# Kernel optimization log

Measured on AMD Instinct MI355X. Metric: run time of the kernel, lower is better.

Reference implementation:

```python
import jax, jax.numpy as jnp
import numpy as np

N_HEAD, D_MODEL, DQ, DK, DV = 16, 1024, 64, 64, 64
B, LQ, LK = 2, 2048, 2048
EPS = 1e-3


def setup_inputs() -> dict:
    key = jax.random.key(0)
    ks = jax.random.split(key, 8)
    v = jax.random.normal(ks[0], (B, LK, D_MODEL), jnp.float32)
    k = jax.random.normal(ks[1], (B, LK, D_MODEL), jnp.float32)
    q = jax.random.normal(ks[2], (B, LQ, D_MODEL), jnp.float32)
    mask = jax.random.randint(ks[3], (B, LQ, LK), 0, 2).astype(bool)
    # xavier_normal for [n_head, d_model, d*]: fan_in=d_model, fan_out=d* (per torch, last two dims)
    def xav(kk, shape):
        std = np.sqrt(2.0 / (shape[-2] + shape[-1]))
        return jax.random.normal(kk, shape, jnp.float32) * std
    w_q = xav(ks[4], (N_HEAD, D_MODEL, DQ))
    w_k = xav(ks[5], (N_HEAD, D_MODEL, DK))
    w_v = xav(ks[6], (N_HEAD, D_MODEL, DV))
    # output linear: torch default init; use uniform(-1/sqrt(fan_in), ..)
    fan_in = N_HEAD * DV
    bound = 1.0 / np.sqrt(fan_in)
    kw, kb = jax.random.split(ks[7])
    w_o = jax.random.uniform(kw, (fan_in, D_MODEL), jnp.float32, -bound, bound)
    b_o = jax.random.uniform(kb, (D_MODEL,), jnp.float32, -bound, bound)
    gamma = jnp.ones((D_MODEL,), jnp.float32)
    beta = jnp.zeros((D_MODEL,), jnp.float32)
    return {"v": v, "k": k, "q": q, "mask": mask, "w_q": w_q, "w_k": w_k,
            "w_v": w_v, "w_o": w_o, "b_o": b_o, "gamma": gamma, "beta": beta}


def _layer_norm(x, gamma, beta):
    mean = jnp.mean(x, axis=-1, keepdims=True)
    # torch.std default is unbiased (ddof=1); eps added to std (not var)
    std = jnp.std(x, axis=-1, keepdims=True, ddof=1)
    return (x - mean) / (std + EPS) * gamma + beta


def reference(v, k, q, mask, w_q, w_k, w_v, w_o, b_o, gamma, beta):
    residual = k  # source uses k as residual
    # per-head projections: [h, b, l, d*]
    qh = jnp.einsum('bld,hde->hble', q, w_q)
    kh = jnp.einsum('bld,hde->hble', k, w_k)
    vh = jnp.einsum('bld,hde->hble', v, w_v)
    scale = 1.0 / np.sqrt(DK)
    scores = jnp.einsum('hbqe,hbke->hbqk', qh, kh) * scale  # [h,b,Lq,Lk]
    scores = jnp.where(mask[None], -jnp.inf, scores)
    attn = jax.nn.softmax(scores, axis=-1)
    out = jnp.einsum('hbqk,hbke->hbqe', attn, vh)  # [h,b,Lq,dv]
    # cat(split(out, batch, dim=0), dim=-1): heads concatenated on last dim
    out = out.transpose(1, 2, 0, 3).reshape(out.shape[1], out.shape[2], -1)
    out = out @ w_o + b_o
    x = out + residual  # dropout is identity in eval
    return _layer_norm(x, gamma, beta)
```

## Files before the change

### kernel.cpp

```cpp
#include <hip/hip_runtime.h>
#include <math.h>

typedef __bf16 bf16_t;
typedef bf16_t bf16x8 __attribute__((ext_vector_type(8)));
typedef float  f32x4  __attribute__((ext_vector_type(4)));
typedef unsigned short u16;
typedef u16 ushortx4 __attribute__((ext_vector_type(4)));
typedef unsigned long long u64;

#define MFMA16(a, b, c) __builtin_amdgcn_mfma_f32_16x16x32_bf16((a), (b), (c), 0, 0, 0)

__device__ __forceinline__ u16 f2bf(float f) {
    unsigned int u = __float_as_uint(f);
    u = (u + 0x7fffu + ((u >> 16) & 1u)) >> 16;
    return (u16)u;
}

__device__ __forceinline__ float bf2f(unsigned int u) {
    return __uint_as_float(u << 16);
}

__device__ __forceinline__ void gld16(const u16* g, u16* l) {
    __builtin_amdgcn_global_load_lds(
        (const __attribute__((address_space(1))) void*)g,
        (__attribute__((address_space(3))) void*)l, 16, 0, 0);
}


__global__ __launch_bounds__(256) void k_prep(const float* __restrict__ q,
                                              const float* __restrict__ k,
                                              const float* __restrict__ v,
                                              const int* __restrict__ mask,
                                              const float* __restrict__ w_q,
                                              const float* __restrict__ w_k,
                                              const float* __restrict__ w_v,
                                              const float* __restrict__ w_o,
                                              u16* __restrict__ qb,
                                              u16* __restrict__ kb,
                                              u16* __restrict__ vb,
                                              u64* __restrict__ mask64,
                                              u16* __restrict__ wqt,
                                              u16* __restrict__ wkt,
                                              u16* __restrict__ wvt,
                                              u16* __restrict__ wot) {
    __shared__ float tile[32][33];
    int bid = blockIdx.x;
    if (bid < 12288) {
        int sel = bid >> 12;
        int i = (bid & 4095) * 256 + threadIdx.x;
        const float* src = sel == 0 ? q : (sel == 1 ? k : v);
        u16* dst = sel == 0 ? qb : (sel == 1 ? kb : vb);
        float4 val = ((const float4*)src)[i];
        ushortx4 r;
        r[0] = f2bf(val.x); r[1] = f2bf(val.y); r[2] = f2bf(val.z); r[3] = f2bf(val.w);
        ((ushortx4*)dst)[i] = r;
    } else if (bid < 20480) {
        int b2 = bid - 12288;
        int ktg = b2 & 7, q4 = (b2 >> 3) & 511, b = b2 >> 12;
        int wave = threadIdx.x >> 6, lane = threadIdx.x & 63;
        int qq = q4 * 4 + wave;
        const int* mp = mask + ((size_t)(b * 2048 + qq)) * 2048 + ktg * 256 + lane;
#pragma unroll
        for (int i = 0; i < 4; ++i) {
            int m = mp[i * 64];
            u64 bal = __ballot(m != 0);
            if (lane == 0) mask64[((size_t)(b * 32 + ktg * 4 + i)) * 2048 + qq] = bal;
        }
    } else {
        int b3 = bid - 20480;
        const float* src;
        u16* dst;
        int r0, c0, C;
        if (b3 < 3072) {
            int x = b3 & 31, y = (b3 >> 5) & 1, z = b3 >> 6;
            int h = z & 15, sel = z >> 4;
            src = (sel == 0 ? w_q : (sel == 1 ? w_k : w_v)) + (size_t)h * 65536;
            dst = (sel == 0 ? wqt : (sel == 1 ? wkt : wvt)) + (size_t)h * 65536;
            r0 = x * 32; c0 = y * 32; C = 64;
        } else {
            int t = b3 - 3072;
            r0 = (t & 31) * 32; c0 = (t >> 5) * 32; C = 1024;
            src = w_o; dst = wot;
        }
        int tx = threadIdx.x & 31, ty = threadIdx.x >> 5;
        const float* s = src + ((size_t)r0) * C + c0;
#pragma unroll
        for (int i = 0; i < 4; ++i) tile[ty + i * 8][tx] = s[(ty + i * 8) * (size_t)C + tx];
        __syncthreads();
        u16* d = dst + ((size_t)c0) * 1024 + r0;
#pragma unroll
        for (int i = 0; i < 4; ++i) d[(ty + i * 8) * 1024 + tx] = f2bf(tile[tx][ty + i * 8]);
    }
}

#define GEMM_CORE(Ablk, Bblk, ACC)                                                    \
    int c0 = wave * 2;                                                                \
    const u16* Ag0 = Ablk + (size_t)(c0 * 16 + l15) * 1024 + quad * 8;                \
    const u16* Ag1 = Ablk + (size_t)((c0 + 1) * 16 + l15) * 1024 + quad * 8;          \
    const u16* Bg0 = Bblk + (size_t)(c0 * 16 + l15) * 1024 + quad * 8;                \
    const u16* Bg1 = Bblk + (size_t)((c0 + 1) * 16 + l15) * 1024 + quad * 8;          \
    gld16(Ag0, As + c0 * 512); gld16(Ag1, As + (c0 + 1) * 512);                       \
    gld16(Bg0, Bs + c0 * 512); gld16(Bg1, Bs + (c0 + 1) * 512);                       \
    __syncthreads();                                                                  \
    int buf = 0;                                                                      \
    for (int ks = 0; ks < 32; ++ks) {                                                 \
        if (ks < 31) {                                                                \
            int k0 = (ks + 1) * 32;                                                   \
            gld16(Ag0 + k0, As + (buf ^ 1) * 4096 + c0 * 512);                        \
            gld16(Ag1 + k0, As + (buf ^ 1) * 4096 + (c0 + 1) * 512);                  \
            gld16(Bg0 + k0, Bs + (buf ^ 1) * 4096 + c0 * 512);                        \
            gld16(Bg1 + k0, Bs + (buf ^ 1) * 4096 + (c0 + 1) * 512);                  \
        }                                                                             \
        bf16x8 af[4], bfr[4];                                                         \
        _Pragma("unroll")                                                             \
        for (int i = 0; i < 4; ++i)                                                   \
            af[i] = *(const bf16x8*)(As + buf * 4096 + (wy * 4 + i) * 512 + lane * 8);\
        _Pragma("unroll")                                                             \
        for (int j = 0; j < 4; ++j)                                                   \
            bfr[j] = *(const bf16x8*)(Bs + buf * 4096 + (wx * 4 + j) * 512 + lane * 8);\
        _Pragma("unroll")                                                             \
        for (int i = 0; i < 4; ++i)                                                   \
            _Pragma("unroll")                                                         \
            for (int j = 0; j < 4; ++j) ACC[i][j] = MFMA16(af[i], bfr[j], ACC[i][j]); \
        __syncthreads();                                                              \
        buf ^= 1;                                                                     \
    }

__global__ __launch_bounds__(256) void k_proj(
    const u16* __restrict__ qb, const u16* __restrict__ kb, const u16* __restrict__ vb,
    const u16* __restrict__ wqt, const u16* __restrict__ wkt, const u16* __restrict__ wvt,
    u16* __restrict__ oq, u16* __restrict__ okh, u16* __restrict__ ovt) {
    __shared__ __align__(16) u16 smem[18432];
    u16* As = smem;
    u16* Bs = smem + 8192;
    int z = blockIdx.y, gx = blockIdx.x;
    int bm, bn;
    const u16 *A, *B;
    if (z == 0)      { bm = gx & 31; bn = gx >> 5; A = qb; B = wqt; }
    else if (z == 1) { bm = gx & 31; bn = gx >> 5; A = kb; B = wkt; }
    else             { bn = gx & 31; bm = gx >> 5; A = wvt; B = vb; }
    A += (size_t)bm * 128 * 1024;
    B += (size_t)bn * 128 * 1024;
    int tid = threadIdx.x, wave = tid >> 6, lane = tid & 63;
    int wy = wave >> 1, wx = wave & 1, l15 = lane & 15, quad = lane >> 4;
    f32x4 acc[4][4] = {};
    GEMM_CORE(A, B, acc)
    u16* ep = smem + wave * 4608;
    float mulf = (z == 0) ? 0.18033688011112042f : 1.0f;
#pragma unroll
    for (int i = 0; i < 4; ++i)
#pragma unroll
        for (int j = 0; j < 4; ++j)
#pragma unroll
            for (int r = 0; r < 4; ++r)
                ep[(i * 16 + quad * 4 + r) * 72 + j * 16 + l15] = f2bf(acc[i][j][r] * mulf);
    int rl = lane >> 3, cg = lane & 7;
    if (z < 2) {
        int hh = bn * 2 + wx;
        int m0 = bm * 128 + wy * 64;
        int bb = m0 >> 11, l0 = m0 & 2047;
        u16* O = (z ? okh : oq) + ((size_t)((hh * 2 + bb) * 2048 + l0)) * 64;
#pragma unroll
        for (int s = 0; s < 8; ++s) {
            int row = s * 8 + rl;
            uint4 v = *(const uint4*)(ep + row * 72 + cg * 8);
            *(uint4*)(O + (size_t)row * 64 + cg * 8) = v;
        }
    } else {
        int m0 = bm * 128 + wy * 64;
        int hh = m0 >> 6;
        int n0 = bn * 128 + wx * 64;
        int bb = n0 >> 11, l0 = n0 & 2047;
        u16* O = ovt + (size_t)(hh * 2 + bb) * 131072 + (size_t)(m0 & 63) * 2048 + l0;
#pragma unroll
        for (int s = 0; s < 8; ++s) {
            int row = s * 8 + rl;
            uint4 v = *(const uint4*)(ep + row * 72 + cg * 8);
            *(uint4*)(O + (size_t)row * 2048 + cg * 8) = v;
        }
    }
}

__global__ __launch_bounds__(256) void k_attn(
    const u16* __restrict__ qh, const u16* __restrict__ kh,
    const u16* __restrict__ vt, const u64* __restrict__ mask64,
    u16* __restrict__ po, float* __restrict__ pl) {
    int hb = blockIdx.x, qt = blockIdx.y, ksp = blockIdx.z;
    int b = hb & 1;
    int tid = threadIdx.x, wave = tid >> 6, lane = tid & 63;
    int l15 = lane & 15, quad = lane >> 4;

    __shared__ __align__(16) u16 Ks[2][4096], Vs[2][4096];
    __shared__ __align__(16) u16 Eb[4][1024];

    int qrow0 = qt * 128 + wave * 32;
    const u16* Qp = qh + ((size_t)(hb * 2048) + qrow0 + l15) * 64 + quad * 8;
    bf16x8 qf[2][2];
    qf[0][0] = *(const bf16x8*)Qp;
    qf[0][1] = *(const bf16x8*)(Qp + 32);
    qf[1][0] = *(const bf16x8*)(Qp + 1024);
    qf[1][1] = *(const bf16x8*)(Qp + 1024 + 32);

    int c0 = wave * 2;
    int rowp = (wave >> 1) * 32 + (l15 >> 2) * 8 + (wave & 1) * 4 + (l15 & 3);
    const u16* Kg0 = kh + (size_t)hb * 131072 + (size_t)ksp * 65536 +
                     (size_t)rowp * 64 + quad * 8;
    const u16* Kg1 = Kg0 + 32;
    const u16* Vg0 = vt + (size_t)hb * 131072 + (size_t)(wave * 16 + l15) * 2048 +
                     ksp * 1024 + quad * 8;
    const u16* Vg1 = Vg0 + 32;
    const u64* Mp = mask64 + (size_t)b * 65536 + (size_t)ksp * 32768 + qrow0 + l15;

    float l_lane[2] = {0.f, 0.f};
    f32x4 o[2][4] = {};

    gld16(Kg0, &Ks[0][c0 * 512]);
    gld16(Kg1, &Ks[0][(c0 + 1) * 512]);
    gld16(Vg0, &Vs[0][c0 * 512]);
    gld16(Vg1, &Vs[0][(c0 + 1) * 512]);
    u64 mw0 = Mp[0], mw1 = Mp[16];
    __syncthreads();
    int buf = 0;
    for (int kt = 0; kt < 16; ++kt) {
        u64 mwn0 = 0, mwn1 = 0;
        if (kt < 15) {
            gld16(Kg0 + (size_t)(kt + 1) * 4096, &Ks[buf ^ 1][c0 * 512]);
            gld16(Kg1 + (size_t)(kt + 1) * 4096, &Ks[buf ^ 1][(c0 + 1) * 512]);
            gld16(Vg0 + (size_t)(kt + 1) * 64, &Vs[buf ^ 1][c0 * 512]);
            gld16(Vg1 + (size_t)(kt + 1) * 64, &Vs[buf ^ 1][(c0 + 1) * 512]);
            mwn0 = Mp[(size_t)(kt + 1) * 2048];
            mwn1 = Mp[(size_t)(kt + 1) * 2048 + 16];
        }
        bf16x8 kf[8], vf[8];
#pragma unroll
        for (int c = 0; c < 8; ++c) kf[c] = *(const bf16x8*)&Ks[buf][c * 512 + lane * 8];
#pragma unroll
        for (int c = 0; c < 8; ++c) vf[c] = *(const bf16x8*)&Vs[buf][c * 512 + lane * 8];
#pragma unroll
        for (int hf = 0; hf < 2; ++hf) {
            u64 mw = hf ? mw1 : mw0;
            f32x4 st[4] = {};
#pragma unroll
            for (int t = 0; t < 4; ++t) {
                st[t] = MFMA16(kf[t * 2], qf[hf][0], st[t]);
                st[t] = MFMA16(kf[t * 2 + 1], qf[hf][1], st[t]);
            }
            unsigned int w0 = (unsigned int)(mw >> (quad * 8));
            unsigned int w1 = (unsigned int)(mw >> (32 + quad * 8));
#pragma unroll
            for (int r = 0; r < 4; ++r) {
                st[0][r] = ((w0 >> r) & 1u) ? -3e30f : st[0][r];
                st[1][r] = ((w0 >> (4 + r)) & 1u) ? -3e30f : st[1][r];
                st[2][r] = ((w1 >> r) & 1u) ? -3e30f : st[2][r];
                st[3][r] = ((w1 >> (4 + r)) & 1u) ? -3e30f : st[3][r];
            }
            float ll = 0.f;
            unsigned int pw[8];
#pragma unroll
            for (int t = 0; t < 4; ++t) {
                float p0 = __builtin_amdgcn_exp2f(st[t][0]);
                float p1 = __builtin_amdgcn_exp2f(st[t][1]);
                float p2 = __builtin_amdgcn_exp2f(st[t][2]);
                float p3 = __builtin_amdgcn_exp2f(st[t][3]);
                ll += (p0 + p1) + (p2 + p3);
                pw[t * 2]     = (__float_as_uint(p1) & 0xffff0000u) | (__float_as_uint(p0) >> 16);
                pw[t * 2 + 1] = (__float_as_uint(p3) & 0xffff0000u) | (__float_as_uint(p2) >> 16);
            }
            l_lane[hf] += ll;
            union { unsigned int w[4]; bf16x8 v; } p0u, p1u;
            p0u.w[0] = pw[0]; p0u.w[1] = pw[1]; p0u.w[2] = pw[2]; p0u.w[3] = pw[3];
            p1u.w[0] = pw[4]; p1u.w[1] = pw[5]; p1u.w[2] = pw[6]; p1u.w[3] = pw[7];
#pragma unroll
            for (int t = 0; t < 4; ++t) {
                o[hf][t] = MFMA16(p0u.v, vf[t * 2], o[hf][t]);
                o[hf][t] = MFMA16(p1u.v, vf[t * 2 + 1], o[hf][t]);
            }
        }
        mw0 = mwn0; mw1 = mwn1;
        __syncthreads();
        buf ^= 1;
    }
    size_t rowbase = ((size_t)ksp * 32 + hb) * 2048 + qrow0;
    int rl = lane >> 3, cg = lane & 7;
#pragma unroll
    for (int hf = 0; hf < 2; ++hf) {
        float ls = l_lane[hf];
        ls += __shfl_xor(ls, 16, 64);
        ls += __shfl_xor(ls, 32, 64);
        if (quad == 0) pl[rowbase + hf * 16 + l15] = ls;
#pragma unroll
        for (int t = 0; t < 4; ++t)
#pragma unroll
            for (int r = 0; r < 4; ++r) {
                int row = quad * 4 + r, col = t * 16 + l15;
                int g = col >> 3;
                Eb[wave][row * 64 + ((g ^ (row & 7)) << 3) + (col & 7)] =
                    f2bf(o[hf][t][r]);
            }
#pragma unroll
        for (int s = 0; s < 2; ++s) {
            int row = s * 8 + rl;
            uint4 v = *(const uint4*)&Eb[wave][row * 64 + ((cg ^ (row & 7)) << 3)];
            *(uint4*)(po + (rowbase + hf * 16 + row) * 64 + cg * 8) = v;
        }
    }
}

__global__ __launch_bounds__(256) void k_amerge(const u16* __restrict__ po,
                                                const float* __restrict__ pl,
                                                u16* __restrict__ ao) {
    int bid = blockIdx.x;
    int hb = bid >> 6, rc = bid & 63;
    int h = hb >> 1, b = hb & 1;
    int tid = threadIdx.x;
    int r = tid >> 3, c = tid & 7;
    int row = rc * 32 + r;
    size_t i0 = ((size_t)hb * 2048 + row) * 64 + c * 8;
    uint4 a0 = *(const uint4*)(po + i0);
    uint4 a1 = *(const uint4*)(po + i0 + 4194304);
    float l0 = pl[(size_t)hb * 2048 + row];
    float l1 = pl[65536 + (size_t)hb * 2048 + row];
    float inv = 1.0f / (l0 + l1);
    unsigned int* pa0 = (unsigned int*)&a0;
    unsigned int* pa1 = (unsigned int*)&a1;
    uint4 out;
    unsigned int* po_ = (unsigned int*)&out;
#pragma unroll
    for (int i = 0; i < 4; ++i) {
        float lo = (bf2f(pa0[i] & 0xffffu) + bf2f(pa1[i] & 0xffffu)) * inv;
        float hi = (bf2f(pa0[i] >> 16) + bf2f(pa1[i] >> 16)) * inv;
        po_[i] = (unsigned int)f2bf(lo) | ((unsigned int)f2bf(hi) << 16);
    }
    *(uint4*)(ao + ((size_t)(b * 2048 + row)) * 1024 + h * 64 + c * 8) = out;
}

__global__ __launch_bounds__(512) void k_out(
    const u16* __restrict__ ao, const u16* __restrict__ wot,
    float* __restrict__ xp0, float* __restrict__ xp1) {
    __shared__ __align__(16) u16 smem[18432];
    u16* As = smem;
    u16* Bs = smem + 8192;
    int gx = blockIdx.x, bm = gx & 31, bn = gx >> 5;
    int ksp = blockIdx.y;
    const u16* A = ao + (size_t)bm * 128 * 1024 + ksp * 512;
    const u16* B = wot + (size_t)bn * 128 * 1024 + ksp * 512;
    float* xp = ksp ? xp1 : xp0;
    int tid = threadIdx.x, wave = tid >> 6, lane = tid & 63;
    int wy = wave >> 2, wx = wave & 3, l15 = lane & 15, quad = lane >> 4;
    const u16* Ag = A + (size_t)(wave * 16 + l15) * 1024 + quad * 8;
    const u16* Bg = B + (size_t)(wave * 16 + l15) * 1024 + quad * 8;
    f32x4 acc[4][2] = {};
    gld16(Ag, As + wave * 512);
    gld16(Bg, Bs + wave * 512);
    __syncthreads();
    int buf = 0;
    for (int ks = 0; ks < 16; ++ks) {
        if (ks < 15) {
            int k0 = (ks + 1) * 32;
            gld16(Ag + k0, As + (buf ^ 1) * 4096 + wave * 512);
            gld16(Bg + k0, Bs + (buf ^ 1) * 4096 + wave * 512);
        }
        bf16x8 af[4], bfr[2];
#pragma unroll
        for (int i = 0; i < 4; ++i)
            af[i] = *(const bf16x8*)(As + buf * 4096 + (wy * 4 + i) * 512 + lane * 8);
#pragma unroll
        for (int j = 0; j < 2; ++j)
            bfr[j] = *(const bf16x8*)(Bs + buf * 4096 + (wx * 2 + j) * 512 + lane * 8);
#pragma unroll
        for (int i = 0; i < 4; ++i)
#pragma unroll
            for (int j = 0; j < 2; ++j) acc[i][j] = MFMA16(af[i], bfr[j], acc[i][j]);
        __syncthreads();
        buf ^= 1;
    }
    float* epf = (float*)smem + wave * 1152;
    int rl = lane >> 3, cg = lane & 7;
    int mbase = bm * 128 + wy * 64, nbase = bn * 128 + wx * 32;
#pragma unroll
    for (int cc = 0; cc < 2; ++cc) {
#pragma unroll
        for (int i2 = 0; i2 < 2; ++i2)
#pragma unroll
            for (int j = 0; j < 2; ++j)
#pragma unroll
                for (int r = 0; r < 4; ++r)
                    epf[(i2 * 16 + quad * 4 + r) * 36 + j * 16 + l15] =
                        acc[cc * 2 + i2][j][r];
#pragma unroll
        for (int s = 0; s < 4; ++s) {
            int row = s * 8 + rl;
            f32x4 v = *(const f32x4*)(epf + row * 36 + cg * 4);
            int m = mbase + cc * 32 + row, n = nbase + cg * 4;
            *(f32x4*)(xp + (size_t)m * 1024 + n) = v;
        }
    }
}

__global__ __launch_bounds__(256) void k_ln(const float* __restrict__ xp0,
                                            const float* __restrict__ xp1,
                                            const float* __restrict__ resid,
                                            const float* __restrict__ bo,
                                            const float* __restrict__ gamma,
                                            const float* __restrict__ beta,
                                            float* __restrict__ out) {
    int row = blockIdx.x;
    size_t base = (size_t)row * 256;
    float4 a0 = ((const float4*)xp0)[base + threadIdx.x];
    float4 a1 = ((const float4*)xp1)[base + threadIdx.x];
    float4 rs = ((const float4*)resid)[base + threadIdx.x];
    float4 b4 = ((const float4*)bo)[threadIdx.x];
    float4 v;
    v.x = a0.x + a1.x + rs.x + b4.x;
    v.y = a0.y + a1.y + rs.y + b4.y;
    v.z = a0.z + a1.z + rs.z + b4.z;
    v.w = a0.w + a1.w + rs.w + b4.w;
    float s = v.x + v.y + v.z + v.w;
    float ss = v.x * v.x + v.y * v.y + v.z * v.z + v.w * v.w;
#pragma unroll
    for (int off = 32; off; off >>= 1) {
        s += __shfl_down(s, off, 64);
        ss += __shfl_down(ss, off, 64);
    }
    __shared__ float sb[8];
    int wave = threadIdx.x >> 6, lane = threadIdx.x & 63;
    if (lane == 0) { sb[wave] = s; sb[4 + wave] = ss; }
    __syncthreads();
    s = sb[0] + sb[1] + sb[2] + sb[3];
    ss = sb[4] + sb[5] + sb[6] + sb[7];
    float mean = s * (1.0f / 1024.0f);
    float var = fmaxf((ss - 1024.0f * mean * mean) * (1.0f / 1023.0f), 0.f);
    float inv = 1.0f / (sqrtf(var) + 1e-3f);
    float4 g = ((const float4*)gamma)[threadIdx.x];
    float4 bt = ((const float4*)beta)[threadIdx.x];
    float4 o;
    o.x = (v.x - mean) * inv * g.x + bt.x;
    o.y = (v.y - mean) * inv * g.y + bt.y;
    o.z = (v.z - mean) * inv * g.z + bt.z;
    o.w = (v.w - mean) * inv * g.w + bt.w;
    ((float4*)(out))[base + threadIdx.x] = o;
}

extern "C" void kernel_launch(void* const* d_in, const int* in_sizes, int n_in,
                              void* d_out, int out_size, void* d_ws, size_t ws_size,
                              hipStream_t stream) {
    const float* v_in  = (const float*)d_in[0];
    const float* k_in  = (const float*)d_in[1];
    const float* q_in  = (const float*)d_in[2];
    const int*   mask  = (const int*)d_in[3];
    const float* w_q   = (const float*)d_in[4];
    const float* w_k   = (const float*)d_in[5];
    const float* w_v   = (const float*)d_in[6];
    const float* w_o   = (const float*)d_in[7];
    const float* b_o   = (const float*)d_in[8];
    const float* gamma = (const float*)d_in[9];
    const float* beta  = (const float*)d_in[10];
    float* out = (float*)d_out;

    char* ws = (char*)d_ws;
    const size_t MB = 1ull << 20;
    u16* qb  = (u16*)(ws + 0 * MB);
    u16* kb  = (u16*)(ws + 8 * MB);
    u16* vb  = (u16*)(ws + 16 * MB);
    u16* wqt = (u16*)(ws + 24 * MB);
    u16* wkt = (u16*)(ws + 26 * MB);
    u16* wvt = (u16*)(ws + 28 * MB);
    u16* wot = (u16*)(ws + 30 * MB);
    u16* qh  = (u16*)(ws + 32 * MB);
    u16* kh  = (u16*)(ws + 40 * MB);
    u16* vt  = (u16*)(ws + 48 * MB);
    u16* ao  = (u16*)(ws + 56 * MB);
    u64* mask64 = (u64*)(ws + 64 * MB);
    u16*   po = (u16*)(ws + 0 * MB);
    float* pl = (float*)(ws + 16 * MB);
    float* xp0 = (float*)(ws + 32 * MB);
    float* xp1 = (float*)(ws + 64 * MB);

    k_prep<<<dim3(24576), dim3(256), 0, stream>>>(q_in, k_in, v_in, mask,
                                                  w_q, w_k, w_v, w_o,
                                                  qb, kb, vb, mask64,
                                                  wqt, wkt, wvt, wot);
    k_proj<<<dim3(256, 3), dim3(256), 0, stream>>>(qb, kb, vb, wqt, wkt, wvt, qh, kh, vt);
    k_attn<<<dim3(32, 16, 2), dim3(256), 0, stream>>>(qh, kh, vt, mask64, po, pl);
    k_amerge<<<dim3(2048), dim3(256), 0, stream>>>(po, pl, ao);
    k_out<<<dim3(256, 2), dim3(512), 0, stream>>>(ao, wot, xp0, xp1);
    k_ln<<<dim3(4096), dim3(256), 0, stream>>>(xp0, xp1, k_in, b_o, gamma, beta, out);
}
```

Before: 293.2 us.

## Precompute mask as per-lane MFMA fragment bitmasks loaded via scalar memory

The mask preprocessing now emits 64-bit ballot words laid out to match the MFMA accumulator layout, one word per score element across the wave. The attention kernel reads them with scalar (constant address space) loads and applies masking with a single v_cndmask using an SGPR lane mask, which removes the per-element shift-and-test VALU work. In exchange the mask buffer becomes larger (16 words per fragment instead of one per row), there are more scalar loads per tile, and the prep kernel issues more ballots.

```diff
diff --git a/kernel.cpp b/kernel.cpp
--- a/kernel.cpp
+++ b/kernel.cpp
@@ -38,7 +38,7 @@
                                               u16* __restrict__ qb,
                                               u16* __restrict__ kb,
                                               u16* __restrict__ vb,
-                                              u64* __restrict__ mask64,
+                                              u64* __restrict__ mfrag,
                                               u16* __restrict__ wqt,
                                               u16* __restrict__ wkt,
                                               u16* __restrict__ wvt,
@@ -54,20 +54,27 @@
         ushortx4 r;
         r[0] = f2bf(val.x); r[1] = f2bf(val.y); r[2] = f2bf(val.z); r[3] = f2bf(val.w);
         ((ushortx4*)dst)[i] = r;
-    } else if (bid < 20480) {
-        int b2 = bid - 12288;
-        int ktg = b2 & 7, q4 = (b2 >> 3) & 511, b = b2 >> 12;
+    } else if (bid < 14336) {
         int wave = threadIdx.x >> 6, lane = threadIdx.x & 63;
-        int qq = q4 * 4 + wave;
-        const int* mp = mask + ((size_t)(b * 2048 + qq)) * 2048 + ktg * 256 + lane;
-#pragma unroll
-        for (int i = 0; i < 4; ++i) {
-            int m = mp[i * 64];
-            u64 bal = __ballot(m != 0);
-            if (lane == 0) mask64[((size_t)(b * 32 + ktg * 4 + i)) * 2048 + qq] = bal;
-        }
+        int l15 = lane & 15, quad = lane >> 4;
+        int wt = (bid - 12288) * 4 + wave;
+        int hf = wt & 1;
+        int g = wt >> 1;
+        int ktile = g & 31, qbi = (g >> 5) & 63, b = g >> 11;
+        int qq = qbi * 32 + hf * 16 + l15;
+        const int* mrow = mask + ((size_t)(b * 2048 + qq)) * 2048 + ktile * 64 + quad * 8;
+        u64 myw = 0;
+#pragma unroll
+        for (int t = 0; t < 4; ++t)
+#pragma unroll
+            for (int r = 0; r < 4; ++r) {
+                int m = mrow[(t >> 1) * 32 + (t & 1) * 4 + r];
+                u64 bal = __ballot(m != 0);
+                if (lane == t * 4 + r) myw = bal;
+            }
+        if (lane < 16) mfrag[(size_t)g * 32 + hf * 16 + lane] = myw;
     } else {
-        int b3 = bid - 20480;
+        int b3 = bid - 14336;
         const float* src;
         u16* dst;
         int r0, c0, C;
@@ -183,7 +190,7 @@
 
 __global__ __launch_bounds__(256) void k_attn(
     const u16* __restrict__ qh, const u16* __restrict__ kh,
-    const u16* __restrict__ vt, const u64* __restrict__ mask64,
+    const u16* __restrict__ vt, const u64* __restrict__ mfrag,
     u16* __restrict__ po, float* __restrict__ pl) {
     int hb = blockIdx.x, qt = blockIdx.y, ksp = blockIdx.z;
     int b = hb & 1;
@@ -209,27 +216,28 @@
     const u16* Vg0 = vt + (size_t)hb * 131072 + (size_t)(wave * 16 + l15) * 2048 +
                      ksp * 1024 + quad * 8;
     const u16* Vg1 = Vg0 + 32;
-    const u64* Mp = mask64 + (size_t)b * 65536 + (size_t)ksp * 32768 + qrow0 + l15;
+
+    int wu = __builtin_amdgcn_readfirstlane(wave);
+    const __attribute__((address_space(4))) u64* Mw =
+        (const __attribute__((address_space(4))) u64*)(mfrag +
+            (size_t)(((b * 64 + qt * 4 + wu) * 32 + ksp * 16) * 32));
 
     float l_lane[2] = {0.f, 0.f};
     f32x4 o[2][4] = {};
+    float neg = -3e30f;
 
     gld16(Kg0, &Ks[0][c0 * 512]);
     gld16(Kg1, &Ks[0][(c0 + 1) * 512]);
     gld16(Vg0, &Vs[0][c0 * 512]);
     gld16(Vg1, &Vs[0][(c0 + 1) * 512]);
-    u64 mw0 = Mp[0], mw1 = Mp[16];
     __syncthreads();
     int buf = 0;
     for (int kt = 0; kt < 16; ++kt) {
-        u64 mwn0 = 0, mwn1 = 0;
         if (kt < 15) {
             gld16(Kg0 + (size_t)(kt + 1) * 4096, &Ks[buf ^ 1][c0 * 512]);
             gld16(Kg1 + (size_t)(kt + 1) * 4096, &Ks[buf ^ 1][(c0 + 1) * 512]);
             gld16(Vg0 + (size_t)(kt + 1) * 64, &Vs[buf ^ 1][c0 * 512]);
             gld16(Vg1 + (size_t)(kt + 1) * 64, &Vs[buf ^ 1][(c0 + 1) * 512]);
-            mwn0 = Mp[(size_t)(kt + 1) * 2048];
-            mwn1 = Mp[(size_t)(kt + 1) * 2048 + 16];
         }
         bf16x8 kf[8], vf[8];
 #pragma unroll
@@ -238,30 +246,32 @@
         for (int c = 0; c < 8; ++c) vf[c] = *(const bf16x8*)&Vs[buf][c * 512 + lane * 8];
 #pragma unroll
         for (int hf = 0; hf < 2; ++hf) {
-            u64 mw = hf ? mw1 : mw0;
+            u64 mw[16];
+#pragma unroll
+            for (int i = 0; i < 16; ++i) mw[i] = Mw[kt * 32 + hf * 16 + i];
             f32x4 st[4] = {};
 #pragma unroll
             for (int t = 0; t < 4; ++t) {
                 st[t] = MFMA16(kf[t * 2], qf[hf][0], st[t]);
                 st[t] = MFMA16(kf[t * 2 + 1], qf[hf][1], st[t]);
             }
-            unsigned int w0 = (unsigned int)(mw >> (quad * 8));
-            unsigned int w1 = (unsigned int)(mw >> (32 + quad * 8));
-#pragma unroll
-            for (int r = 0; r < 4; ++r) {
-                st[0][r] = ((w0 >> r) & 1u) ? -3e30f : st[0][r];
-                st[1][r] = ((w0 >> (4 + r)) & 1u) ? -3e30f : st[1][r];
-                st[2][r] = ((w1 >> r) & 1u) ? -3e30f : st[2][r];
-                st[3][r] = ((w1 >> (4 + r)) & 1u) ? -3e30f : st[3][r];
-            }
+            float p[16];
+#pragma unroll
+            for (int t = 0; t < 4; ++t)
+#pragma unroll
+                for (int r = 0; r < 4; ++r) {
+                    float sc;
+                    asm("v_cndmask_b32 %0, %1, %2, %3"
+                        : "=v"(sc)
+                        : "v"(st[t][r]), "v"(neg), "s"(mw[t * 4 + r]));
+                    p[t * 4 + r] = __builtin_amdgcn_exp2f(sc);
+                }
             float ll = 0.f;
             unsigned int pw[8];
 #pragma unroll
             for (int t = 0; t < 4; ++t) {
-                float p0 = __builtin_amdgcn_exp2f(st[t][0]);
-                float p1 = __builtin_amdgcn_exp2f(st[t][1]);
-                float p2 = __builtin_amdgcn_exp2f(st[t][2]);
-                float p3 = __builtin_amdgcn_exp2f(st[t][3]);
+                float p0 = p[t * 4 + 0], p1 = p[t * 4 + 1];
+                float p2 = p[t * 4 + 2], p3 = p[t * 4 + 3];
                 ll += (p0 + p1) + (p2 + p3);
                 pw[t * 2]     = (__float_as_uint(p1) & 0xffff0000u) | (__float_as_uint(p0) >> 16);
                 pw[t * 2 + 1] = (__float_as_uint(p3) & 0xffff0000u) | (__float_as_uint(p2) >> 16);
@@ -276,7 +286,6 @@
                 o[hf][t] = MFMA16(p1u.v, vf[t * 2 + 1], o[hf][t]);
             }
         }
-        mw0 = mwn0; mw1 = mwn1;
         __syncthreads();
         buf ^= 1;
     }
@@ -470,18 +479,18 @@
     u16* kh  = (u16*)(ws + 40 * MB);
     u16* vt  = (u16*)(ws + 48 * MB);
     u16* ao  = (u16*)(ws + 56 * MB);
-    u64* mask64 = (u64*)(ws + 64 * MB);
+    u64* mfrag = (u64*)(ws + 64 * MB);
     u16*   po = (u16*)(ws + 0 * MB);
     float* pl = (float*)(ws + 16 * MB);
     float* xp0 = (float*)(ws + 32 * MB);
     float* xp1 = (float*)(ws + 64 * MB);
 
-    k_prep<<<dim3(24576), dim3(256), 0, stream>>>(q_in, k_in, v_in, mask,
+    k_prep<<<dim3(18432), dim3(256), 0, stream>>>(q_in, k_in, v_in, mask,
                                                   w_q, w_k, w_v, w_o,
-                                                  qb, kb, vb, mask64,
+                                                  qb, kb, vb, mfrag,
                                                   wqt, wkt, wvt, wot);
     k_proj<<<dim3(256, 3), dim3(256), 0, stream>>>(qb, kb, vb, wqt, wkt, wvt, qh, kh, vt);
-    k_attn<<<dim3(32, 16, 2), dim3(256), 0, stream>>>(qh, kh, vt, mask64, po, pl);
+    k_attn<<<dim3(32, 16, 2), dim3(256), 0, stream>>>(qh, kh, vt, mfrag, po, pl);
     k_amerge<<<dim3(2048), dim3(256), 0, stream>>>(po, pl, ao);
     k_out<<<dim3(256, 2), dim3(512), 0, stream>>>(ao, wot, xp0, xp1);
     k_ln<<<dim3(4096), dim3(256), 0, stream>>>(xp0, xp1, k_in, b_o, gamma, beta, out);
```

Measured after the change: 287.5 us. Within noise of the previous version (-1.9%).
